# Optimization experiments

Hardware: AMD Instinct MI355X
Metric: run time of the kernel (lower is better)

## Reference

```python
import jax, jax.numpy as jnp
import numpy as np

WS = 7          # window size
DISP = 3        # WS // 2 cyclic shift displacement
HEADS = 3
HD = 32         # head dim
DIM = 96        # hidden dim (= HEADS*HD)
DS = 4          # patch-merging downscale factor
NWH = 16        # windows per spatial dim after merging (112/7)
SCALE = HD ** -0.5


def _rel_indices(ws):
    idx = np.array([[x, y] for x in range(ws) for y in range(ws)])
    return idx[None, :, :] - idx[:, None, :] + ws - 1  # (ws^2, ws^2, 2)


def _shift_mask(ws, disp, nwh, nww):
    n = ws * ws
    ul = np.zeros((n, n), np.float32)
    ul[-disp * ws:, :-disp * ws] = -np.inf
    ul[:-disp * ws, -disp * ws:] = -np.inf
    lr = np.zeros((ws, ws, ws, ws), np.float32)
    lr[:, -disp:, :, :-disp] = -np.inf
    lr[:, :-disp, :, -disp:] = -np.inf
    lr = lr.reshape(n, n)
    m = np.zeros((nwh * nww, n, n), np.float32)
    m[-nww:] += ul            # last row of windows: upper/lower mask
    m[nww - 1::nww] += lr     # last column of windows: left/right mask
    return m

REL = jnp.asarray(_rel_indices(WS))                       # (49,49,2) int
SHIFT_MASK = jnp.asarray(_shift_mask(WS, DISP, NWH, NWH))  # (256,49,49)


def _layernorm(x, g, b):
    mu = jnp.mean(x, axis=-1, keepdims=True)
    var = jnp.var(x, axis=-1, keepdims=True)
    return (x - mu) * jax.lax.rsqrt(var + 1e-5) * g + b


def _window_attention(y, wqkv, pos_tab, wo, bo, shifted):
    # y: (b, nh, nw, DIM)
    if shifted:
        y = jnp.roll(y, (-DISP, -DISP), axis=(1, 2))
    b, nh, nw, _ = y.shape
    nwh, nww = nh // WS, nw // WS
    qkv = y @ wqkv  # (b, nh, nw, 3*DIM); last dim layout [q|k|v]
    qkv = qkv.reshape(b, nwh, WS, nww, WS, 3, HEADS, HD)
    qkv = qkv.transpose(5, 0, 6, 1, 3, 2, 4, 7).reshape(3, b, HEADS, nwh * nww, WS * WS, HD)
    q, k, v = qkv[0], qkv[1], qkv[2]
    dots = jnp.einsum('bhwid,bhwjd->bhwij', q, k) * SCALE  # (b,h,nwin,49,49)
    dots = dots + pos_tab[REL[..., 0], REL[..., 1]]        # relative pos bias
    if shifted:
        dots = dots + SHIFT_MASK[None, None]
    attn = jax.nn.softmax(dots, axis=-1)
    o = jnp.einsum('bhwij,bhwjd->bhwid', attn, v)
    o = o.reshape(b, HEADS, nwh, nww, WS, WS, HD)
    o = o.transpose(0, 2, 4, 3, 5, 1, 6).reshape(b, nh, nw, HEADS * HD)
    o = o @ wo + bo
    if shifted:
        o = jnp.roll(o, (DISP, DISP), axis=(1, 2))
    return o


def setup_inputs() -> dict:
    key = jax.random.key(0)
    ks = jax.random.split(key, 8)
    B, C, H, W = 16, 3, 448, 448
    s = 0.02
    return {
        'x': jax.random.normal(ks[0], (B, C, H, W), jnp.float32),
        'pm_w': jax.random.normal(ks[1], (C * DS * DS, DIM), jnp.float32) * s,
        'pm_b': jnp.zeros((DIM,), jnp.float32),
        'ln1_g': jnp.ones((2, DIM), jnp.float32),
        'ln1_b': jnp.zeros((2, DIM), jnp.float32),
        'qkv_w': jax.random.normal(ks[2], (2, DIM, 3 * HEADS * HD), jnp.float32) * s,
        'pos': jax.random.normal(ks[3], (2, 2 * WS - 1, 2 * WS - 1), jnp.float32),
        'out_w': jax.random.normal(ks[4], (2, HEADS * HD, DIM), jnp.float32) * s,
        'out_b': jnp.zeros((2, DIM), jnp.float32),
        'ln2_g': jnp.ones((2, DIM), jnp.float32),
        'ln2_b': jnp.zeros((2, DIM), jnp.float32),
        'ff1_w': jax.random.normal(ks[5], (2, DIM, 4 * DIM), jnp.float32) * s,
        'ff1_b': jnp.zeros((2, 4 * DIM), jnp.float32),
        'ff2_w': jax.random.normal(ks[6], (2, 4 * DIM, DIM), jnp.float32) * s,
        'ff2_b': jnp.zeros((2, DIM), jnp.float32),
    }


def reference(x, pm_w, pm_b, ln1_g, ln1_b, qkv_w, pos, out_w, out_b,
              ln2_g, ln2_b, ff1_w, ff1_b, ff2_w, ff2_b):
    b, c, h, w = x.shape
    # PatchMerging: Unfold(k=s=DS) orders channels as (c, kh, kw)
    xp = x.reshape(b, c, h // DS, DS, w // DS, DS)
    xp = xp.transpose(0, 2, 4, 1, 3, 5).reshape(b, h // DS, w // DS, c * DS * DS)
    xp = xp @ pm_w + pm_b  # (b, 112, 112, DIM)
    for i, shifted in enumerate((False, True)):
        y = _layernorm(xp, ln1_g[i], ln1_b[i])
        xp = xp + _window_attention(y, qkv_w[i], pos[i], out_w[i], out_b[i], shifted)
        y = _layernorm(xp, ln2_g[i], ln2_b[i])
        y = jax.nn.gelu(y @ ff1_w[i] + ff1_b[i], approximate=False) @ ff2_w[i] + ff2_b[i]
        xp = xp + y
    return xp.transpose(0, 3, 1, 2)  # (b, DIM, 112, 112)
```

## Files before the change

### kernel.cpp

```cpp
#include <hip/hip_runtime.h>
#include <hip/hip_bf16.h>

#define HW 112
#define NPIX (HW*HW)
#define NTOK_TOTAL (16*NPIX)
#define SCALE_ATTN 0.17677669529663689f

typedef short bf16x8 __attribute__((ext_vector_type(8)));
typedef float f32x4 __attribute__((ext_vector_type(4)));

__device__ __forceinline__ short f2bf(float f) {
    __hip_bfloat16 h = __float2bfloat16(f);
    return *reinterpret_cast<short*>(&h);
}

__device__ __forceinline__ float gelu_tanh(float x) {
    float t  = x * x;
    float m1 = fmaf(0.071354816f, t, 1.5957691f);
    float e  = __expf(x * m1);
    float r  = __builtin_amdgcn_rcpf(e + 1.0f);
    return fmaf(-x, r, x);
}

__device__ __forceinline__ void gload_lds16(const short* g, short* l) {
    __builtin_amdgcn_global_load_lds(
        (__attribute__((address_space(1))) void*)g,
        (__attribute__((address_space(3))) void*)l,
        16, 0, 0);
}

__global__ __launch_bounds__(256) void patch_merge_kernel(
    const float* __restrict__ x, const float* __restrict__ pm_w,
    const float* __restrict__ pm_b, float* __restrict__ xp)
{
    __shared__ float w_lds[48*96];
    __shared__ float in_lds[16*52];
    __shared__ float b_lds[96];
    const int t = threadIdx.x;
    const int jt = blockIdx.x, i = blockIdx.y, b = blockIdx.z;
    const int j0 = jt * 16;

    for (int e = t; e < 48*96; e += 256) w_lds[e] = pm_w[e];
    if (t < 96) b_lds[t] = pm_b[t];
    for (int e = t; e < 768; e += 256) {
        int r = e >> 6, col = e & 63;
        int c = r >> 2, kh = r & 3;
        float v = x[(((size_t)(b*3 + c))*448 + (4*i + kh))*448 + 4*j0 + col];
        in_lds[(col >> 2)*52 + c*16 + kh*4 + (col & 3)] = v;
    }
    __syncthreads();
    for (int e = t; e < 16*96; e += 256) {
        int pos = e / 96, ch = e % 96;
        float acc = b_lds[ch];
        #pragma unroll
        for (int k = 0; k < 48; ++k)
            acc = fmaf(in_lds[pos*52 + k], w_lds[k*96 + ch], acc);
        xp[((size_t)((b*HW + i)*HW) + j0 + pos)*96 + ch] = acc;
    }
}

__global__ __launch_bounds__(256) void prep_weights_kernel(
    const float* __restrict__ ff1, const float* __restrict__ ff2,
    const float* __restrict__ qkv_w, const float* __restrict__ out_w,
    short* __restrict__ wF,
    short* __restrict__ qkvT, short* __restrict__ outT)
{
    int i = blockIdx.x * 256 + threadIdx.x;
    if (i < 147456) {
        int l = i / 73728, r = i % 73728;
        int c = r / 18432, r2 = r % 18432;
        int half = r2 / 9216, r3 = r2 % 9216;
        int f = r3 / 512, L = (r3 % 512) / 8, j = r3 % 8;
        int ks = f / 6, n = f % 6;
        float val;
        if (half == 0) {
            int k  = ks*32 + (L >> 4)*8 + j;
            int ng = c*96 + n*16 + (L & 15);
            val = ff1[(size_t)l*36864 + (size_t)k*384 + ng];
        } else {
            int kg = c*96 + ks*32 + (L >> 4)*8 + j;
            int ng = n*16 + (L & 15);
            val = ff2[(size_t)l*36864 + (size_t)kg*96 + ng];
        }
        wF[i] = f2bf(val);
    } else if (i < 202752) {
        int j = i - 147456;
        int l = j / 27648, r = j % 27648, n = r / 96, k = r % 96;
        qkvT[j] = f2bf(qkv_w[(size_t)l*27648 + k*288 + n]);
    } else if (i < 221184) {
        int j = i - 202752;
        int l = j / 9216, r = j % 9216, n = r / 96, k = r % 96;
        outT[j] = f2bf(out_w[(size_t)l*9216 + k*96 + n]);
    }
}

template<bool SHIFTED>
__global__ __launch_bounds__(192) void attn_mfma_kernel(
    float* __restrict__ xp,
    const float* __restrict__ ln_g, const float* __restrict__ ln_b,
    const short* __restrict__ qkvT,
    const float* __restrict__ pos_tab,
    const short* __restrict__ outT,
    const float* __restrict__ out_b)
{
    __shared__ short bufA[13824];
    __shared__ short qk_s[13824];
    __shared__ short vT_s[6912];
    __shared__ float pos_l[169];
    __shared__ float ob_s[96];
    __shared__ float lng[96], lnb[96];

    const int t = threadIdx.x;
    const int lane = t & 63;
    const int h = t >> 6;
    const int l15 = lane & 15, lhi = lane >> 4;
    const int wh = blockIdx.x >> 4, ww = blockIdx.x & 15;
    const int b = blockIdx.y;
    const int SH = SHIFTED ? 3 : 0;

    if (t < 169) pos_l[t] = pos_tab[t];
    if (t < 96) { lng[t] = ln_g[t]; lnb[t] = ln_b[t]; ob_s[t] = out_b[t]; }
    __syncthreads();

    {
        const int part = t & 3;
        for (int row = t >> 2; row < 49; row += 48) {
            int ti = (row*37) >> 8, tj = row - ti*7;
            int gi = wh*7 + ti + SH; if (gi >= HW) gi -= HW;
            int gj = ww*7 + tj + SH; if (gj >= HW) gj -= HW;
            const float* src = xp + ((size_t)((b*HW + gi)*HW + gj))*96 + part*24;
            float v[24];
            #pragma unroll
            for (int q4 = 0; q4 < 6; ++q4) {
                float4 vv = *reinterpret_cast<const float4*>(src + q4*4);
                v[q4*4+0]=vv.x; v[q4*4+1]=vv.y; v[q4*4+2]=vv.z; v[q4*4+3]=vv.w;
            }
            float s = 0.f, s2 = 0.f;
            #pragma unroll
            for (int j = 0; j < 24; ++j) { s += v[j]; s2 += v[j]*v[j]; }
            s  += __shfl_xor(s, 1);  s  += __shfl_xor(s, 2);
            s2 += __shfl_xor(s2, 1); s2 += __shfl_xor(s2, 2);
            float mu = s * (1.f/96.f);
            float var = s2 * (1.f/96.f) - mu*mu;
            float rs = rsqrtf(var + 1e-5f);
            unsigned* yw = reinterpret_cast<unsigned*>(bufA) + row*52 + part*12;
            #pragma unroll
            for (int j = 0; j < 12; ++j) {
                int c = part*24 + 2*j;
                float lo = (v[2*j]   - mu)*rs*lng[c]   + lnb[c];
                float hi = (v[2*j+1] - mu)*rs*lng[c+1] + lnb[c+1];
                yw[j] = (unsigned)(unsigned short)f2bf(lo) |
                        ((unsigned)(unsigned short)f2bf(hi) << 16);
            }
        }
        for (int e = t; e < 15*52; e += 192)
            reinterpret_cast<unsigned*>(bufA)[(49 + e/52)*52 + e%52] = 0u;
    }
    __syncthreads();

    {
        f32x4 acc[3][2][4];
        #pragma unroll
        for (int p = 0; p < 3; ++p)
            #pragma unroll
            for (int s = 0; s < 2; ++s)
                #pragma unroll
                for (int m = 0; m < 4; ++m)
                    { acc[p][s][m][0]=0.f; acc[p][s][m][1]=0.f; acc[p][s][m][2]=0.f; acc[p][s][m][3]=0.f; }
        #pragma unroll
        for (int ks = 0; ks < 3; ++ks) {
            bf16x8 a[4];
            #pragma unroll
            for (int m = 0; m < 4; ++m)
                a[m] = *reinterpret_cast<const bf16x8*>(&bufA[(m*16 + l15)*104 + ks*32 + lhi*8]);
            #pragma unroll
            for (int p = 0; p < 3; ++p)
                #pragma unroll
                for (int s = 0; s < 2; ++s) {
                    bf16x8 bf = *reinterpret_cast<const bf16x8*>(
                        qkvT + (p*96 + h*32 + s*16 + l15)*96 + ks*32 + lhi*8);
                    #pragma unroll
                    for (int m = 0; m < 4; ++m)
                        acc[p][s][m] = __builtin_amdgcn_mfma_f32_16x16x32_bf16(
                            a[m], bf, acc[p][s][m], 0, 0, 0);
                }
        }
        #pragma unroll
        for (int p = 0; p < 3; ++p)
            #pragma unroll
            for (int s = 0; s < 2; ++s)
                #pragma unroll
                for (int m = 0; m < 4; ++m)
                    #pragma unroll
                    for (int r = 0; r < 4; ++r) {
                        int tok = m*16 + lhi*4 + r;
                        int c = s*16 + l15;
                        short val = f2bf(acc[p][s][m][r]);
                        if (p == 0)      qk_s[h*4608 + tok*72 + c] = val;
                        else if (p == 1) qk_s[h*4608 + tok*72 + 32 + c] = val;
                        else             vT_s[h*2304 + c*72 + tok] = val;
                    }
    }
    __syncthreads();

    float pv[4][4][4];
    {
        f32x4 sacc[4][4];
        #pragma unroll
        for (int m = 0; m < 4; ++m)
            #pragma unroll
            for (int n = 0; n < 4; ++n)
                { sacc[m][n][0]=0.f; sacc[m][n][1]=0.f; sacc[m][n][2]=0.f; sacc[m][n][3]=0.f; }
        bf16x8 aq[4], bk[4];
        #pragma unroll
        for (int m = 0; m < 4; ++m)
            aq[m] = *reinterpret_cast<const bf16x8*>(&qk_s[h*4608 + (m*16 + l15)*72 + lhi*8]);
        #pragma unroll
        for (int n = 0; n < 4; ++n)
            bk[n] = *reinterpret_cast<const bf16x8*>(&qk_s[h*4608 + (n*16 + l15)*72 + 32 + lhi*8]);
        #pragma unroll
        for (int m = 0; m < 4; ++m)
            #pragma unroll
            for (int n = 0; n < 4; ++n)
                sacc[m][n] = __builtin_amdgcn_mfma_f32_16x16x32_bf16(aq[m], bk[n], sacc[m][n], 0, 0, 0);

        #pragma unroll
        for (int m = 0; m < 4; ++m)
            #pragma unroll
            for (int n = 0; n < 4; ++n)
                #pragma unroll
                for (int r = 0; r < 4; ++r) {
                    int i = m*16 + lhi*4 + r, j = n*16 + l15;
                    float v;
                    if (i >= 49 || j >= 49) v = -1e30f;
                    else {
                        int xi = (i*37) >> 8, yi = i - xi*7;
                        int xj = (j*37) >> 8, yj = j - xj*7;
                        v = sacc[m][n][r]*SCALE_ATTN + pos_l[(xj - xi + 6)*13 + (yj - yi + 6)];
                        if (SHIFTED) {
                            if (wh == 15 && ((xi >= 4) != (xj >= 4))) v = -1e30f;
                            if (ww == 15 && ((yi >= 4) != (yj >= 4))) v = -1e30f;
                        }
                    }
                    pv[m][n][r] = v;
                }
    }
    #pragma unroll
    for (int m = 0; m < 4; ++m)
        #pragma unroll
        for (int r = 0; r < 4; ++r) {
            float mx = fmaxf(fmaxf(pv[m][0][r], pv[m][1][r]), fmaxf(pv[m][2][r], pv[m][3][r]));
            mx = fmaxf(mx, __shfl_xor(mx, 1)); mx = fmaxf(mx, __shfl_xor(mx, 2));
            mx = fmaxf(mx, __shfl_xor(mx, 4)); mx = fmaxf(mx, __shfl_xor(mx, 8));
            float e0 = __expf(pv[m][0][r] - mx), e1 = __expf(pv[m][1][r] - mx);
            float e2 = __expf(pv[m][2][r] - mx), e3 = __expf(pv[m][3][r] - mx);
            float s = e0 + e1 + e2 + e3;
            s += __shfl_xor(s, 1); s += __shfl_xor(s, 2);
            s += __shfl_xor(s, 4); s += __shfl_xor(s, 8);
            float inv = 1.f / s;
            pv[m][0][r] = e0*inv; pv[m][1][r] = e1*inv;
            pv[m][2][r] = e2*inv; pv[m][3][r] = e3*inv;
        }
    #pragma unroll
    for (int m = 0; m < 4; ++m)
        #pragma unroll
        for (int n = 0; n < 4; ++n)
            #pragma unroll
            for (int r = 0; r < 4; ++r)
                bufA[h*4608 + (m*16 + lhi*4 + r)*72 + n*16 + l15] = f2bf(pv[m][n][r]);

    f32x4 oacc[2][4];
    #pragma unroll
    for (int n = 0; n < 2; ++n)
        #pragma unroll
        for (int m = 0; m < 4; ++m)
            { oacc[n][m][0]=0.f; oacc[n][m][1]=0.f; oacc[n][m][2]=0.f; oacc[n][m][3]=0.f; }
    #pragma unroll
    for (int ks = 0; ks < 2; ++ks) {
        bf16x8 ap[4], bv[2];
        #pragma unroll
        for (int m = 0; m < 4; ++m)
            ap[m] = *reinterpret_cast<const bf16x8*>(&bufA[h*4608 + (m*16 + l15)*72 + ks*32 + lhi*8]);
        #pragma unroll
        for (int n = 0; n < 2; ++n)
            bv[n] = *reinterpret_cast<const bf16x8*>(&vT_s[h*2304 + (n*16 + l15)*72 + ks*32 + lhi*8]);
        #pragma unroll
        for (int n = 0; n < 2; ++n)
            #pragma unroll
            for (int m = 0; m < 4; ++m)
                oacc[n][m] = __builtin_amdgcn_mfma_f32_16x16x32_bf16(ap[m], bv[n], oacc[n][m], 0, 0, 0);
    }
    __syncthreads();
    #pragma unroll
    for (int n = 0; n < 2; ++n)
        #pragma unroll
        for (int m = 0; m < 4; ++m)
            #pragma unroll
            for (int r = 0; r < 4; ++r)
                bufA[(m*16 + lhi*4 + r)*104 + h*32 + n*16 + l15] = f2bf(oacc[n][m][r]);
    __syncthreads();

    {
        f32x4 pacc[2][4];
        #pragma unroll
        for (int n = 0; n < 2; ++n)
            #pragma unroll
            for (int m = 0; m < 4; ++m)
                { pacc[n][m][0]=0.f; pacc[n][m][1]=0.f; pacc[n][m][2]=0.f; pacc[n][m][3]=0.f; }
        #pragma unroll
        for (int ks = 0; ks < 3; ++ks) {
            bf16x8 ao[4], bw[2];
            #pragma unroll
            for (int m = 0; m < 4; ++m)
                ao[m] = *reinterpret_cast<const bf16x8*>(&bufA[(m*16 + l15)*104 + ks*32 + lhi*8]);
            #pragma unroll
            for (int n = 0; n < 2; ++n)
                bw[n] = *reinterpret_cast<const bf16x8*>(
                    outT + ((h*2 + n)*16 + l15)*96 + ks*32 + lhi*8);
            #pragma unroll
            for (int n = 0; n < 2; ++n)
                #pragma unroll
                for (int m = 0; m < 4; ++m)
                    pacc[n][m] = __builtin_amdgcn_mfma_f32_16x16x32_bf16(ao[m], bw[n], pacc[n][m], 0, 0, 0);
        }
        #pragma unroll
        for (int m = 0; m < 4; ++m)
            #pragma unroll
            for (int r = 0; r < 4; ++r) {
                int tok = m*16 + lhi*4 + r;
                if (tok < 49) {
                    int ti = (tok*37) >> 8, tj = tok - ti*7;
                    int gi = wh*7 + ti + SH; if (gi >= HW) gi -= HW;
                    int gj = ww*7 + tj + SH; if (gj >= HW) gj -= HW;
                    float* dst = xp + ((size_t)((b*HW + gi)*HW + gj))*96;
                    #pragma unroll
                    for (int n = 0; n < 2; ++n) {
                        int ch = (h*2 + n)*16 + l15;
                        dst[ch] += pacc[n][m][r] + ob_s[ch];
                    }
                }
            }
    }
}

__global__ __launch_bounds__(256) void ff_mfma_kernel(
    float* __restrict__ xp,
    const float* __restrict__ ln_g, const float* __restrict__ ln_b,
    const short* __restrict__ wF,
    const float* __restrict__ b1,
    const float* __restrict__ b2)
{
    __shared__ short wbuf[18432];
    __shared__ short h_s[128*104];

    const int t = threadIdx.x;
    const int lane = t & 63;
    const int wv = t >> 6;
    const int l15 = lane & 15, lhi = (lane >> 4) & 3;
    const size_t tok0 = (size_t)blockIdx.x * 128 + wv*32;

    #pragma unroll
    for (int k = 0; k < 9; ++k) {
        int f = k*4 + wv;
        gload_lds16(wF + f*512 + lane*8, &wbuf[f*512]);
    }

    bf16x8 y[2][3];
    {
        float g[24], bb[24];
        #pragma unroll
        for (int ks = 0; ks < 3; ++ks)
            #pragma unroll
            for (int q = 0; q < 2; ++q) {
                float4 gv = *reinterpret_cast<const float4*>(ln_g + ks*32 + lhi*8 + q*4);
                float4 bv = *reinterpret_cast<const float4*>(ln_b + ks*32 + lhi*8 + q*4);
                g[ks*8+q*4+0]=gv.x; g[ks*8+q*4+1]=gv.y; g[ks*8+q*4+2]=gv.z; g[ks*8+q*4+3]=gv.w;
                bb[ks*8+q*4+0]=bv.x; bb[ks*8+q*4+1]=bv.y; bb[ks*8+q*4+2]=bv.z; bb[ks*8+q*4+3]=bv.w;
            }
        #pragma unroll
        for (int m = 0; m < 2; ++m) {
            const float* src = xp + (tok0 + m*16 + l15)*96 + lhi*8;
            float v[24];
            #pragma unroll
            for (int ks = 0; ks < 3; ++ks) {
                float4 a0 = *reinterpret_cast<const float4*>(src + ks*32);
                float4 a1 = *reinterpret_cast<const float4*>(src + ks*32 + 4);
                v[ks*8+0]=a0.x; v[ks*8+1]=a0.y; v[ks*8+2]=a0.z; v[ks*8+3]=a0.w;
                v[ks*8+4]=a1.x; v[ks*8+5]=a1.y; v[ks*8+6]=a1.z; v[ks*8+7]=a1.w;
            }
            float s = 0.f, s2 = 0.f;
            #pragma unroll
            for (int j = 0; j < 24; ++j) { s += v[j]; s2 += v[j]*v[j]; }
            s  += __shfl_xor(s, 16);  s  += __shfl_xor(s, 32);
            s2 += __shfl_xor(s2, 16); s2 += __shfl_xor(s2, 32);
            float mu = s * (1.f/96.f);
            float var = s2 * (1.f/96.f) - mu*mu;
            float rs = rsqrtf(var + 1e-5f);
            #pragma unroll
            for (int ks = 0; ks < 3; ++ks) {
                bf16x8 yy;
                #pragma unroll
                for (int j = 0; j < 8; ++j)
                    yy[j] = f2bf((v[ks*8+j] - mu)*rs*g[ks*8+j] + bb[ks*8+j]);
                y[m][ks] = yy;
            }
        }
    }

    f32x4 acc2[2][6];
    #pragma unroll
    for (int m = 0; m < 2; ++m)
        #pragma unroll
        for (int n = 0; n < 6; ++n)
            { acc2[m][n][0]=0.f; acc2[m][n][1]=0.f; acc2[m][n][2]=0.f; acc2[m][n][3]=0.f; }

    asm volatile("s_waitcnt vmcnt(0)" ::: "memory");
    __syncthreads();

    for (int c = 0; c < 4; ++c) {
        f32x4 acc1[2][6];
        #pragma unroll
        for (int m = 0; m < 2; ++m)
            #pragma unroll
            for (int n = 0; n < 6; ++n)
                { acc1[m][n][0]=0.f; acc1[m][n][1]=0.f; acc1[m][n][2]=0.f; acc1[m][n][3]=0.f; }
        #pragma unroll
        for (int ks = 0; ks < 3; ++ks)
            #pragma unroll
            for (int n = 0; n < 6; ++n) {
                bf16x8 bw = *reinterpret_cast<const bf16x8*>(
                    &wbuf[(ks*6 + n)*512 + lane*8]);
                #pragma unroll
                for (int m = 0; m < 2; ++m)
                    acc1[m][n] = __builtin_amdgcn_mfma_f32_16x16x32_bf16(
                        y[m][ks], bw, acc1[m][n], 0, 0, 0);
            }

        #pragma unroll
        for (int n = 0; n < 6; ++n) {
            float bias = b1[c*96 + n*16 + l15];
            #pragma unroll
            for (int m = 0; m < 2; ++m)
                #pragma unroll
                for (int r = 0; r < 4; ++r) {
                    float hv = gelu_tanh(acc1[m][n][r] + bias);
                    int row = wv*32 + m*16 + lhi*4 + r;
                    h_s[row*104 + n*16 + l15] = f2bf(hv);
                }
        }

        #pragma unroll
        for (int ks = 0; ks < 3; ++ks) {
            bf16x8 ah[2];
            #pragma unroll
            for (int m = 0; m < 2; ++m)
                ah[m] = *reinterpret_cast<const bf16x8*>(
                    &h_s[(wv*32 + m*16 + l15)*104 + ks*32 + lhi*8]);
            #pragma unroll
            for (int n = 0; n < 6; ++n) {
                bf16x8 bw = *reinterpret_cast<const bf16x8*>(
                    &wbuf[9216 + (ks*6 + n)*512 + lane*8]);
                #pragma unroll
                for (int m = 0; m < 2; ++m)
                    acc2[m][n] = __builtin_amdgcn_mfma_f32_16x16x32_bf16(
                        ah[m], bw, acc2[m][n], 0, 0, 0);
            }
        }

        if (c < 3) {
            __syncthreads();
            #pragma unroll
            for (int k = 0; k < 9; ++k) {
                int f = k*4 + wv;
                gload_lds16(wF + (c + 1)*18432 + f*512 + lane*8, &wbuf[f*512]);
            }
            asm volatile("s_waitcnt vmcnt(0)" ::: "memory");
            __syncthreads();
        }
    }

    float b2v[6];
    #pragma unroll
    for (int n = 0; n < 6; ++n) b2v[n] = b2[n*16 + l15];
    #pragma unroll
    for (int m = 0; m < 2; ++m)
        #pragma unroll
        for (int r = 0; r < 4; ++r) {
            float* dst = xp + (tok0 + m*16 + lhi*4 + r)*96 + l15;
            #pragma unroll
            for (int n = 0; n < 6; ++n)
                dst[n*16] += acc2[m][n][r] + b2v[n];
        }
}

__global__ __launch_bounds__(256) void out_kernel(
    const float* __restrict__ xp, float* __restrict__ out)
{
    __shared__ float tile[64*100];
    const int t = threadIdx.x;
    const int b = blockIdx.y;
    const int p0 = blockIdx.x * 64;
    for (int e = t; e < 64*24; e += 256) {
        int r = e / 24, p = e % 24;
        *reinterpret_cast<float4*>(&tile[r*100 + p*4]) =
            *reinterpret_cast<const float4*>(xp + ((size_t)b*NPIX + p0 + r)*96 + p*4);
    }
    __syncthreads();
    for (int e = t; e < 96*64; e += 256) {
        int ch = e >> 6, p = e & 63;
        out[((size_t)(b*96 + ch))*NPIX + p0 + p] = tile[p*100 + ch];
    }
}

extern "C" void kernel_launch(void* const* d_in, const int* in_sizes, int n_in,
                              void* d_out, int out_size, void* d_ws, size_t ws_size,
                              hipStream_t stream)
{
    (void)in_sizes; (void)n_in; (void)out_size; (void)ws_size;
    const float* x     = (const float*)d_in[0];
    const float* pm_w  = (const float*)d_in[1];
    const float* pm_b  = (const float*)d_in[2];
    const float* ln1_g = (const float*)d_in[3];
    const float* ln1_b = (const float*)d_in[4];
    const float* qkv_w = (const float*)d_in[5];
    const float* pos   = (const float*)d_in[6];
    const float* out_w = (const float*)d_in[7];
    const float* out_b = (const float*)d_in[8];
    const float* ln2_g = (const float*)d_in[9];
    const float* ln2_b = (const float*)d_in[10];
    const float* ff1_w = (const float*)d_in[11];
    const float* ff1_b = (const float*)d_in[12];
    const float* ff2_w = (const float*)d_in[13];
    const float* ff2_b = (const float*)d_in[14];

    float* xp    = (float*)d_ws;
    short* wF_b  = (short*)(xp + (size_t)NTOK_TOTAL * 96);
    short* qkvT_b = wF_b + 147456;
    short* outT_b = qkvT_b + 2*288*96;

    prep_weights_kernel<<<864, 256, 0, stream>>>(ff1_w, ff2_w, qkv_w, out_w,
                                                 wF_b, qkvT_b, outT_b);
    patch_merge_kernel<<<dim3(7, 112, 16), 256, 0, stream>>>(x, pm_w, pm_b, xp);

    for (int L = 0; L < 2; ++L) {
        if (L == 0)
            attn_mfma_kernel<false><<<dim3(256, 16), 192, 0, stream>>>(
                xp, ln1_g, ln1_b, qkvT_b, pos, outT_b, out_b);
        else
            attn_mfma_kernel<true><<<dim3(256, 16), 192, 0, stream>>>(
                xp, ln1_g + 96, ln1_b + 96, qkvT_b + 27648, pos + 169,
                outT_b + 9216, out_b + 96);
        ff_mfma_kernel<<<1568, 256, 0, stream>>>(
            xp, ln2_g + L*96, ln2_b + L*96,
            wF_b + (size_t)L*73728, ff1_b + L*384, ff2_b + L*96);
    }
    out_kernel<<<dim3(196, 16), 256, 0, stream>>>(xp, (float*)d_out);
}
```

Measured before the change: 523.0 us.

## Shrink attention LDS, fold scale into Q weights, precompute 49x49 position bias

The attention kernel now computes V after QK^T and softmax, reusing the LN input buffer, so the separate V-transpose LDS buffer goes away and bufA is halved. The goal is a smaller LDS footprint and fewer live accumulators, allowing 4 blocks per CU. The attention scale is folded into the Q weights during weight prep. The relative position bias is expanded once into a padded 49x52 table, removing per-element index arithmetic, and s_setprio hints are placed around the MFMA loops. The expanded bias table adds about 10KB of LDS per block, and the V projection becomes a separate later phase.

```diff
diff --git a/kernel.cpp b/kernel.cpp
--- a/kernel.cpp
+++ b/kernel.cpp
@@ -62,8 +62,9 @@
 __global__ __launch_bounds__(256) void prep_weights_kernel(
     const float* __restrict__ ff1, const float* __restrict__ ff2,
     const float* __restrict__ qkv_w, const float* __restrict__ out_w,
-    short* __restrict__ wF,
-    short* __restrict__ qkvT, short* __restrict__ outT)
+    const float* __restrict__ pos,
+    short* __restrict__ wF, short* __restrict__ qkvT,
+    short* __restrict__ outT, float* __restrict__ pos49)
 {
     int i = blockIdx.x * 256 + threadIdx.x;
     if (i < 147456) {
@@ -86,27 +87,37 @@
     } else if (i < 202752) {
         int j = i - 147456;
         int l = j / 27648, r = j % 27648, n = r / 96, k = r % 96;
-        qkvT[j] = f2bf(qkv_w[(size_t)l*27648 + k*288 + n]);
+        float v = qkv_w[(size_t)l*27648 + k*288 + n];
+        if (n < 96) v *= SCALE_ATTN;
+        qkvT[j] = f2bf(v);
     } else if (i < 221184) {
         int j = i - 202752;
         int l = j / 9216, r = j % 9216, n = r / 96, k = r % 96;
         outT[j] = f2bf(out_w[(size_t)l*9216 + k*96 + n]);
+    } else if (i < 226280) {
+        int j = i - 221184;
+        int l = j / 2548, r = j % 2548, ti = r / 52, tj = r % 52;
+        float v = 0.f;
+        if (ti < 49 && tj < 49) {
+            int xi = ti / 7, yi = ti % 7, xj = tj / 7, yj = tj % 7;
+            v = pos[l*169 + (xj - xi + 6)*13 + (yj - yi + 6)];
+        }
+        pos49[j] = v;
     }
 }
 
 template<bool SHIFTED>
-__global__ __launch_bounds__(192) void attn_mfma_kernel(
+__global__ __launch_bounds__(192, 4) void attn_mfma_kernel(
     float* __restrict__ xp,
     const float* __restrict__ ln_g, const float* __restrict__ ln_b,
     const short* __restrict__ qkvT,
-    const float* __restrict__ pos_tab,
+    const float* __restrict__ pos49,
     const short* __restrict__ outT,
     const float* __restrict__ out_b)
 {
-    __shared__ short bufA[13824];
+    __shared__ short bufA[6912];
     __shared__ short qk_s[13824];
-    __shared__ short vT_s[6912];
-    __shared__ float pos_l[169];
+    __shared__ float pos_l[2548];
     __shared__ float ob_s[96];
     __shared__ float lng[96], lnb[96];
 
@@ -118,7 +129,7 @@
     const int b = blockIdx.y;
     const int SH = SHIFTED ? 3 : 0;
 
-    if (t < 169) pos_l[t] = pos_tab[t];
+    for (int e = t; e < 2548; e += 192) pos_l[e] = pos49[e];
     if (t < 96) { lng[t] = ln_g[t]; lnb[t] = ln_b[t]; ob_s[t] = out_b[t]; }
     __syncthreads();
 
@@ -159,14 +170,15 @@
     __syncthreads();
 
     {
-        f32x4 acc[3][2][4];
-        #pragma unroll
-        for (int p = 0; p < 3; ++p)
+        f32x4 acc[2][2][4];
+        #pragma unroll
+        for (int p = 0; p < 2; ++p)
             #pragma unroll
             for (int s = 0; s < 2; ++s)
                 #pragma unroll
                 for (int m = 0; m < 4; ++m)
                     { acc[p][s][m][0]=0.f; acc[p][s][m][1]=0.f; acc[p][s][m][2]=0.f; acc[p][s][m][3]=0.f; }
+        __builtin_amdgcn_s_setprio(1);
         #pragma unroll
         for (int ks = 0; ks < 3; ++ks) {
             bf16x8 a[4];
@@ -174,7 +186,7 @@
             for (int m = 0; m < 4; ++m)
                 a[m] = *reinterpret_cast<const bf16x8*>(&bufA[(m*16 + l15)*104 + ks*32 + lhi*8]);
             #pragma unroll
-            for (int p = 0; p < 3; ++p)
+            for (int p = 0; p < 2; ++p)
                 #pragma unroll
                 for (int s = 0; s < 2; ++s) {
                     bf16x8 bf = *reinterpret_cast<const bf16x8*>(
@@ -185,44 +197,41 @@
                             a[m], bf, acc[p][s][m], 0, 0, 0);
                 }
         }
-        #pragma unroll
-        for (int p = 0; p < 3; ++p)
+        __builtin_amdgcn_s_setprio(0);
+        #pragma unroll
+        for (int p = 0; p < 2; ++p)
             #pragma unroll
             for (int s = 0; s < 2; ++s)
                 #pragma unroll
                 for (int m = 0; m < 4; ++m)
                     #pragma unroll
-                    for (int r = 0; r < 4; ++r) {
-                        int tok = m*16 + lhi*4 + r;
-                        int c = s*16 + l15;
-                        short val = f2bf(acc[p][s][m][r]);
-                        if (p == 0)      qk_s[h*4608 + tok*72 + c] = val;
-                        else if (p == 1) qk_s[h*4608 + tok*72 + 32 + c] = val;
-                        else             vT_s[h*2304 + c*72 + tok] = val;
-                    }
-    }
-    __syncthreads();
+                    for (int r = 0; r < 4; ++r)
+                        qk_s[h*4608 + (m*16 + lhi*4 + r)*72 + p*32 + s*16 + l15] =
+                            f2bf(acc[p][s][m][r]);
+    }
 
     float pv[4][4][4];
     {
+        bf16x8 aq[4], bk[4];
+        #pragma unroll
+        for (int m = 0; m < 4; ++m)
+            aq[m] = *reinterpret_cast<const bf16x8*>(&qk_s[h*4608 + (m*16 + l15)*72 + lhi*8]);
+        #pragma unroll
+        for (int n = 0; n < 4; ++n)
+            bk[n] = *reinterpret_cast<const bf16x8*>(&qk_s[h*4608 + (n*16 + l15)*72 + 32 + lhi*8]);
         f32x4 sacc[4][4];
         #pragma unroll
         for (int m = 0; m < 4; ++m)
             #pragma unroll
             for (int n = 0; n < 4; ++n)
                 { sacc[m][n][0]=0.f; sacc[m][n][1]=0.f; sacc[m][n][2]=0.f; sacc[m][n][3]=0.f; }
-        bf16x8 aq[4], bk[4];
-        #pragma unroll
-        for (int m = 0; m < 4; ++m)
-            aq[m] = *reinterpret_cast<const bf16x8*>(&qk_s[h*4608 + (m*16 + l15)*72 + lhi*8]);
-        #pragma unroll
-        for (int n = 0; n < 4; ++n)
-            bk[n] = *reinterpret_cast<const bf16x8*>(&qk_s[h*4608 + (n*16 + l15)*72 + 32 + lhi*8]);
+        __builtin_amdgcn_s_setprio(1);
         #pragma unroll
         for (int m = 0; m < 4; ++m)
             #pragma unroll
             for (int n = 0; n < 4; ++n)
                 sacc[m][n] = __builtin_amdgcn_mfma_f32_16x16x32_bf16(aq[m], bk[n], sacc[m][n], 0, 0, 0);
+        __builtin_amdgcn_s_setprio(0);
 
         #pragma unroll
         for (int m = 0; m < 4; ++m)
@@ -234,12 +243,16 @@
                     float v;
                     if (i >= 49 || j >= 49) v = -1e30f;
                     else {
-                        int xi = (i*37) >> 8, yi = i - xi*7;
-                        int xj = (j*37) >> 8, yj = j - xj*7;
-                        v = sacc[m][n][r]*SCALE_ATTN + pos_l[(xj - xi + 6)*13 + (yj - yi + 6)];
+                        v = sacc[m][n][r] + pos_l[i*52 + j];
                         if (SHIFTED) {
-                            if (wh == 15 && ((xi >= 4) != (xj >= 4))) v = -1e30f;
-                            if (ww == 15 && ((yi >= 4) != (yj >= 4))) v = -1e30f;
+                            if (wh == 15) {
+                                int xi = (i*37) >> 8, xj = (j*37) >> 8;
+                                if ((xi >= 4) != (xj >= 4)) v = -1e30f;
+                            }
+                            if (ww == 15) {
+                                int yi = i - ((i*37) >> 8)*7, yj = j - ((j*37) >> 8)*7;
+                                if ((yi >= 4) != (yj >= 4)) v = -1e30f;
+                            }
                         }
                     }
                     pv[m][n][r] = v;
@@ -267,7 +280,40 @@
         for (int n = 0; n < 4; ++n)
             #pragma unroll
             for (int r = 0; r < 4; ++r)
-                bufA[h*4608 + (m*16 + lhi*4 + r)*72 + n*16 + l15] = f2bf(pv[m][n][r]);
+                qk_s[h*4608 + (m*16 + lhi*4 + r)*72 + n*16 + l15] = f2bf(pv[m][n][r]);
+
+    f32x4 vacc[2][4];
+    #pragma unroll
+    for (int s = 0; s < 2; ++s)
+        #pragma unroll
+        for (int m = 0; m < 4; ++m)
+            { vacc[s][m][0]=0.f; vacc[s][m][1]=0.f; vacc[s][m][2]=0.f; vacc[s][m][3]=0.f; }
+    __builtin_amdgcn_s_setprio(1);
+    #pragma unroll
+    for (int ks = 0; ks < 3; ++ks) {
+        bf16x8 a[4];
+        #pragma unroll
+        for (int m = 0; m < 4; ++m)
+            a[m] = *reinterpret_cast<const bf16x8*>(&bufA[(m*16 + l15)*104 + ks*32 + lhi*8]);
+        #pragma unroll
+        for (int s = 0; s < 2; ++s) {
+            bf16x8 bf = *reinterpret_cast<const bf16x8*>(
+                qkvT + (192 + h*32 + s*16 + l15)*96 + ks*32 + lhi*8);
+            #pragma unroll
+            for (int m = 0; m < 4; ++m)
+                vacc[s][m] = __builtin_amdgcn_mfma_f32_16x16x32_bf16(
+                    a[m], bf, vacc[s][m], 0, 0, 0);
+        }
+    }
+    __builtin_amdgcn_s_setprio(0);
+    __syncthreads();
+    #pragma unroll
+    for (int s = 0; s < 2; ++s)
+        #pragma unroll
+        for (int m = 0; m < 4; ++m)
+            #pragma unroll
+            for (int r = 0; r < 4; ++r)
+                bufA[h*2304 + (s*16 + l15)*72 + m*16 + lhi*4 + r] = f2bf(vacc[s][m][r]);
 
     f32x4 oacc[2][4];
     #pragma unroll
@@ -275,21 +321,23 @@
         #pragma unroll
         for (int m = 0; m < 4; ++m)
             { oacc[n][m][0]=0.f; oacc[n][m][1]=0.f; oacc[n][m][2]=0.f; oacc[n][m][3]=0.f; }
+    __builtin_amdgcn_s_setprio(1);
     #pragma unroll
     for (int ks = 0; ks < 2; ++ks) {
         bf16x8 ap[4], bv[2];
         #pragma unroll
         for (int m = 0; m < 4; ++m)
-            ap[m] = *reinterpret_cast<const bf16x8*>(&bufA[h*4608 + (m*16 + l15)*72 + ks*32 + lhi*8]);
+            ap[m] = *reinterpret_cast<const bf16x8*>(&qk_s[h*4608 + (m*16 + l15)*72 + ks*32 + lhi*8]);
         #pragma unroll
         for (int n = 0; n < 2; ++n)
-            bv[n] = *reinterpret_cast<const bf16x8*>(&vT_s[h*2304 + (n*16 + l15)*72 + ks*32 + lhi*8]);
+            bv[n] = *reinterpret_cast<const bf16x8*>(&bufA[h*2304 + (n*16 + l15)*72 + ks*32 + lhi*8]);
         #pragma unroll
         for (int n = 0; n < 2; ++n)
             #pragma unroll
             for (int m = 0; m < 4; ++m)
                 oacc[n][m] = __builtin_amdgcn_mfma_f32_16x16x32_bf16(ap[m], bv[n], oacc[n][m], 0, 0, 0);
     }
+    __builtin_amdgcn_s_setprio(0);
     __syncthreads();
     #pragma unroll
     for (int n = 0; n < 2; ++n)
@@ -307,6 +355,7 @@
             #pragma unroll
             for (int m = 0; m < 4; ++m)
                 { pacc[n][m][0]=0.f; pacc[n][m][1]=0.f; pacc[n][m][2]=0.f; pacc[n][m][3]=0.f; }
+        __builtin_amdgcn_s_setprio(1);
         #pragma unroll
         for (int ks = 0; ks < 3; ++ks) {
             bf16x8 ao[4], bw[2];
@@ -323,6 +372,7 @@
                 for (int m = 0; m < 4; ++m)
                     pacc[n][m] = __builtin_amdgcn_mfma_f32_16x16x32_bf16(ao[m], bw[n], pacc[n][m], 0, 0, 0);
         }
+        __builtin_amdgcn_s_setprio(0);
         #pragma unroll
         for (int m = 0; m < 4; ++m)
             #pragma unroll
@@ -533,22 +583,23 @@
     const float* ff2_w = (const float*)d_in[13];
     const float* ff2_b = (const float*)d_in[14];
 
-    float* xp    = (float*)d_ws;
-    short* wF_b  = (short*)(xp + (size_t)NTOK_TOTAL * 96);
+    float* xp     = (float*)d_ws;
+    short* wF_b   = (short*)(xp + (size_t)NTOK_TOTAL * 96);
     short* qkvT_b = wF_b + 147456;
     short* outT_b = qkvT_b + 2*288*96;
-
-    prep_weights_kernel<<<864, 256, 0, stream>>>(ff1_w, ff2_w, qkv_w, out_w,
-                                                 wF_b, qkvT_b, outT_b);
+    float* pos49_b = (float*)(outT_b + 2*96*96);
+
+    prep_weights_kernel<<<884, 256, 0, stream>>>(ff1_w, ff2_w, qkv_w, out_w, pos,
+                                                 wF_b, qkvT_b, outT_b, pos49_b);
     patch_merge_kernel<<<dim3(7, 112, 16), 256, 0, stream>>>(x, pm_w, pm_b, xp);
 
     for (int L = 0; L < 2; ++L) {
         if (L == 0)
             attn_mfma_kernel<false><<<dim3(256, 16), 192, 0, stream>>>(
-                xp, ln1_g, ln1_b, qkvT_b, pos, outT_b, out_b);
+                xp, ln1_g, ln1_b, qkvT_b, pos49_b, outT_b, out_b);
         else
             attn_mfma_kernel<true><<<dim3(256, 16), 192, 0, stream>>>(
-                xp, ln1_g + 96, ln1_b + 96, qkvT_b + 27648, pos + 169,
+                xp, ln1_g + 96, ln1_b + 96, qkvT_b + 27648, pos49_b + 2548,
                 outT_b + 9216, out_b + 96);
         ff_mfma_kernel<<<1568, 256, 0, stream>>>(
             xp, ln2_g + L*96, ln2_b + L*96,
```

Result: slower. 551.7 us (+5.5%).
